# Kernel optimization log

Hardware: AMD Instinct MI355X
Metric: run time of the kernel (lower is better)

Reference implementation:

```python
import jax, jax.numpy as jnp
import numpy as np

B, D, M = 512, 1024, 32768
K, MULTI_K, AUX_K = 32, 128, 64
DEAD_THRESH = 256
MATRYOSHKA_SIZES = [4096, 16384, 32768]


def setup_inputs() -> dict:
    key = jax.random.key(0)
    k0, k1, k2, k3, k4, k5 = jax.random.split(key, 6)
    return {
        "x": jax.random.normal(k0, (B, D), dtype=jnp.float32),
        "W_enc": jax.random.normal(k1, (M, D), dtype=jnp.float32) * 0.02,
        "W_dec": jax.random.normal(k2, (D, M), dtype=jnp.float32) * 0.02,
        "input_bias": jax.random.normal(k3, (D,), dtype=jnp.float32) * 0.01,
        "neuron_bias": jax.random.normal(k4, (M,), dtype=jnp.float32) * 0.01,
        "steps_since_activation": jax.random.randint(k5, (M,), 0, 512, dtype=jnp.int64),
    }


def reference(x, W_enc, W_dec, input_bias, neuron_bias, steps_since_activation):
    xc = x - input_bias                                   # [B, D]
    pre_act = xc @ W_enc.T + neuron_bias                  # [B, M]

    topk_values, topk_indices = jax.lax.top_k(pre_act, K)
    topk_values = jax.nn.relu(topk_values)
    multik_values, multik_indices = jax.lax.top_k(pre_act, MULTI_K)
    multik_values = jax.nn.relu(multik_values)

    rows = jnp.arange(pre_act.shape[0])[:, None]
    activations = jnp.zeros_like(pre_act).at[rows, topk_indices].set(topk_values)
    multik_activations = jnp.zeros_like(pre_act).at[rows, multik_indices].set(multik_values)

    reconstruction = activations @ W_dec.T + input_bias
    multik_reconstruction = multik_activations @ W_dec.T + input_bias

    # matryoshka partial reconstructions (all sizes except the last/full one)
    neuron_ids = jnp.arange(M)
    matryoshka_recons = []
    for m_i in MATRYOSHKA_SIZES[:-1]:
        partial_acts = activations * (neuron_ids < m_i).astype(activations.dtype)
        matryoshka_recons.append(partial_acts @ W_dec.T + input_bias)

    # aux-k over dead neurons (steps incremented by 1 before the mask in torch)
    dead_mask = ((steps_since_activation + 1) > DEAD_THRESH).astype(pre_act.dtype)
    aux_values, aux_indices = jax.lax.top_k(pre_act * dead_mask, AUX_K)
    aux_values = jax.nn.relu(aux_values)

    return (reconstruction, multik_reconstruction,
            matryoshka_recons[0], matryoshka_recons[1],
            topk_indices, topk_values, aux_indices, aux_values)
```

## Files before the change

kernel.cpp:

```cpp
#include <hip/hip_runtime.h>
#include <stdint.h>

#define B_ 512
#define D_ 1024
#define M_ 32768

typedef _Float16 half8 __attribute__((ext_vector_type(8)));
typedef _Float16 half4 __attribute__((ext_vector_type(4)));
typedef float f32x4 __attribute__((ext_vector_type(4)));

__device__ __forceinline__ unsigned f2k(float f) {
    unsigned b = __float_as_uint(f);
    return (b & 0x80000000u) ? ~b : (b | 0x80000000u);
}
__device__ __forceinline__ float k2f(unsigned k) {
    unsigned b = (k & 0x80000000u) ? (k & 0x7FFFFFFFu) : ~k;
    return __uint_as_float(b);
}
__device__ __forceinline__ unsigned long long d2k(double d) {
    unsigned long long b = (unsigned long long)__double_as_longlong(d);
    return (b & 0x8000000000000000ull) ? ~b : (b | 0x8000000000000000ull);
}

__device__ __forceinline__ void gld16(const void* g, void* l) {
    __builtin_amdgcn_global_load_lds(
        (__attribute__((address_space(1))) void*)(uintptr_t)g,
        (__attribute__((address_space(3))) void*)(unsigned)(uintptr_t)l,
        16, 0, 0);
}

__global__ __launch_bounds__(256) void split_x_k(
    const float* __restrict__ x, const float* __restrict__ ib,
    _Float16* __restrict__ xh)
{
    int i = blockIdx.x * 256 + threadIdx.x;
    float4 v = ((const float4*)x)[i];
    float4 bb = ((const float4*)ib)[i & 255];
    float a0 = (v.x - bb.x) * 2048.0f;
    float a1 = (v.y - bb.y) * 2048.0f;
    float a2 = (v.z - bb.z) * 2048.0f;
    float a3 = (v.w - bb.w) * 2048.0f;
    half4 hv = {(_Float16)a0, (_Float16)a1, (_Float16)a2, (_Float16)a3};
    ((half4*)xh)[i] = hv;
}

__global__ __launch_bounds__(256, 3) void enc_tr(
    const _Float16* __restrict__ xhf,
    const float* __restrict__ wenc, const float* __restrict__ nb,
    _Float16* __restrict__ preact,
    const float* __restrict__ wdec, _Float16* __restrict__ wdt)
{
    __shared__ alignas(16) char smem[32768];

    const int tid = threadIdx.x;
    const int chunk = blockIdx.x >> 8;

    if (chunk % 3 != 0) {
        const int sub = (chunk - 1 - chunk / 3) * 256 + (blockIdx.x & 255);
        float* tile = (float*)smem;
        const int r = tid >> 2;
        const int q4 = (tid & 3) * 16;
        for (int s = 0; s < 4; ++s) {
            int tix = sub * 4 + s;
            int x0 = (tix & 511) * 64;
            int y0 = (tix >> 9) * 64;
            const float* src = wdec + (size_t)(y0 + r) * M_ + x0 + q4;
            float4 v0 = *(const float4*)(src + 0);
            float4 v1 = *(const float4*)(src + 4);
            float4 v2 = *(const float4*)(src + 8);
            float4 v3 = *(const float4*)(src + 12);
            float* dst = &tile[r * 65 + q4];
            dst[0] = v0.x;  dst[1] = v0.y;  dst[2] = v0.z;  dst[3] = v0.w;
            dst[4] = v1.x;  dst[5] = v1.y;  dst[6] = v1.z;  dst[7] = v1.w;
            dst[8] = v2.x;  dst[9] = v2.y;  dst[10] = v2.z; dst[11] = v2.w;
            dst[12] = v3.x; dst[13] = v3.y; dst[14] = v3.z; dst[15] = v3.w;
            __syncthreads();
            half8 h0, h1;
#pragma unroll
            for (int i = 0; i < 8; ++i) h0[i] = (_Float16)tile[(q4 + i) * 65 + r];
#pragma unroll
            for (int i = 0; i < 8; ++i) h1[i] = (_Float16)tile[(q4 + 8 + i) * 65 + r];
            _Float16* od = wdt + (size_t)(x0 + r) * D_ + y0 + q4;
            *(half8*)(od + 0) = h0;
            *(half8*)(od + 8) = h1;
            __syncthreads();
        }
        return;
    }

    _Float16* lA0 = (_Float16*)smem;
    _Float16* lB0 = (_Float16*)(smem + 16384);

    const int sub = (chunk / 3) * 256 + (blockIdx.x & 255);
    const int lane = tid & 63;
    const int wv = tid >> 6;
    const int wvr = wv >> 1;
    const int wvc = wv & 1;

    const int lb = sub >> 3;
    const int j0 = ((sub & 7) * 32 + (lb >> 2)) * 128;
    const int i0 = (lb & 3) * 128;

    const int ln15 = lane & 15;
    const int kq = (lane >> 4) * 8;

    f32x4 acc1[4][4];
#pragma unroll
    for (int r = 0; r < 4; ++r)
#pragma unroll
        for (int c = 0; c < 4; ++c)
            acc1[r][c] = (f32x4){0.f, 0.f, 0.f, 0.f};

    const int o0 = tid * 16;
    const int o1 = o0 + 4096;
    const int rA0 = o0 >> 6, rA1 = o1 >> 6;
    const int cA0s = (o0 & 63) ^ (((rA0 >> 1) & 3) << 4);
    const int cA1s = (o1 & 63) ^ (((rA1 >> 1) & 3) << 4);

    const int rW = tid >> 1;
    const int c16 = (tid & 1) * 16;
    const int sw = ((rW >> 1) & 3) << 3;
    const int g0 = c16 ^ sw;
    const int g1 = (c16 + 8) ^ sw;

    const int rowA = wvr * 64 + ln15;
    const int rowB = wvc * 64 + ln15;

#define STAGEA(k0, s)                                                                      \
    do {                                                                                   \
        gld16((const char*)(xhf + (size_t)(i0 + rA0) * 1024 + (k0)) + cA0s, (char*)lA0 + (s) * 8192 + o0); \
        gld16((const char*)(xhf + (size_t)(i0 + rA1) * 1024 + (k0)) + cA1s, (char*)lA0 + (s) * 8192 + o1); \
    } while (0)

#define LOADB(k0)                                                                          \
    do {                                                                                   \
        const float* wp = wenc + (size_t)(j0 + rW) * 1024 + (k0) + c16;                    \
        wv0 = *(const float4*)wp;                                                          \
        wv1 = *(const float4*)(wp + 4);                                                    \
        wv2 = *(const float4*)(wp + 8);                                                    \
        wv3 = *(const float4*)(wp + 12);                                                   \
    } while (0)

#define WRITEB(s)                                                                          \
    do {                                                                                   \
        half8 b0, b1;                                                                      \
        b0[0] = (_Float16)(wv0.x * 2048.0f); b0[1] = (_Float16)(wv0.y * 2048.0f);          \
        b0[2] = (_Float16)(wv0.z * 2048.0f); b0[3] = (_Float16)(wv0.w * 2048.0f);          \
        b0[4] = (_Float16)(wv1.x * 2048.0f); b0[5] = (_Float16)(wv1.y * 2048.0f);          \
        b0[6] = (_Float16)(wv1.z * 2048.0f); b0[7] = (_Float16)(wv1.w * 2048.0f);          \
        b1[0] = (_Float16)(wv2.x * 2048.0f); b1[1] = (_Float16)(wv2.y * 2048.0f);          \
        b1[2] = (_Float16)(wv2.z * 2048.0f); b1[3] = (_Float16)(wv2.w * 2048.0f);          \
        b1[4] = (_Float16)(wv3.x * 2048.0f); b1[5] = (_Float16)(wv3.y * 2048.0f);          \
        b1[6] = (_Float16)(wv3.z * 2048.0f); b1[7] = (_Float16)(wv3.w * 2048.0f);          \
        *(half8*)&lB0[(s) * 4096 + rW * 32 + g0] = b0;                                     \
        *(half8*)&lB0[(s) * 4096 + rW * 32 + g1] = b1;                                     \
    } while (0)

    float4 wv0, wv1, wv2, wv3;
    LOADB(0);
    asm volatile("s_waitcnt vmcnt(0)" ::: "memory");
    WRITEB(0);
    STAGEA(0, 0);
    LOADB(32);
    STAGEA(32, 1);
    asm volatile("s_waitcnt vmcnt(2)" ::: "memory");
    WRITEB(1);
    asm volatile("s_waitcnt lgkmcnt(0)" ::: "memory");
    __builtin_amdgcn_s_barrier();

    int cur = 0;
    for (int k0 = 0; k0 < 1024; k0 += 32) {
        if (k0 + 64 < 1024) LOADB(k0 + 64);

        half8 aH[4], bH[4];
#pragma unroll
        for (int r = 0; r < 4; ++r) {
            const int ra = rowA + r * 16;
            const int ka = kq ^ (((ra >> 1) & 3) << 3);
            aH[r] = *(const half8*)&lA0[cur * 4096 + ra * 32 + ka];
        }
#pragma unroll
        for (int c = 0; c < 4; ++c) {
            const int rb = rowB + c * 16;
            const int kb = kq ^ (((rb >> 1) & 3) << 3);
            bH[c] = *(const half8*)&lB0[cur * 4096 + rb * 32 + kb];
        }
#pragma unroll
        for (int r = 0; r < 4; ++r)
#pragma unroll
            for (int c = 0; c < 4; ++c)
                acc1[r][c] = __builtin_amdgcn_mfma_f32_16x16x32_f16(aH[r], bH[c], acc1[r][c], 0, 0, 0);

        if (k0 + 32 < 1024) {
            asm volatile("s_waitcnt lgkmcnt(0)" ::: "memory");
            __builtin_amdgcn_s_barrier();

            if (k0 + 64 < 1024) {
                STAGEA(k0 + 64, cur);
                asm volatile("s_waitcnt vmcnt(2)" ::: "memory");
                WRITEB(cur);
            } else {
                asm volatile("s_waitcnt vmcnt(0)" ::: "memory");
            }
            asm volatile("s_waitcnt lgkmcnt(0)" ::: "memory");
            __builtin_amdgcn_s_barrier();
        }
        cur ^= 1;
    }
#undef STAGEA
#undef LOADB
#undef WRITEB

    asm volatile("s_waitcnt lgkmcnt(0)" ::: "memory");
    __builtin_amdgcn_s_barrier();
    _Float16* ct = (_Float16*)smem;
    const float s1 = 0x1p-22f;
#pragma unroll
    for (int c = 0; c < 4; ++c) {
        int n = wvc * 64 + c * 16 + ln15;
        float nbv = nb[j0 + n];
#pragma unroll
        for (int r = 0; r < 4; ++r) {
            int mb = wvr * 64 + r * 16 + (lane >> 4) * 4;
#pragma unroll
            for (int e = 0; e < 4; ++e)
                ct[(mb + e) * 128 + n] = (_Float16)(acc1[r][c][e] * s1 + nbv);
        }
    }
    __syncthreads();
#pragma unroll
    for (int s = 0; s < 8; ++s) {
        int idx = s * 256 + tid;
        int row = idx >> 4;
        int off8 = (idx & 15) * 8;
        *(half8*)(preact + (size_t)(i0 + row) * M_ + j0 + off8) = *(half8*)&ct[row * 128 + off8];
    }
}

__global__ __launch_bounds__(1024, 2) void selresdec(
    const _Float16* __restrict__ preact, const int* __restrict__ steps,
    const float* __restrict__ x, const float* __restrict__ ib,
    const float* __restrict__ wenc, const float* __restrict__ nb,
    const _Float16* __restrict__ wdt,
    float* __restrict__ out_tidx, float* __restrict__ out_tval,
    float* __restrict__ out_aidx, float* __restrict__ out_aval,
    float* __restrict__ o_recon, float* __restrict__ o_multik,
    float* __restrict__ o_mat0, float* __restrict__ o_mat1)
{
    __shared__ unsigned histU[4096];
    __shared__ unsigned histM[4096];
    __shared__ unsigned coarseU[256];
    __shared__ unsigned coarseM[256];
    __shared__ unsigned long long candU[512];
    __shared__ unsigned long long candM[512];
    __shared__ double xcs[1024];
    __shared__ double part[128][8];
    __shared__ unsigned long long kU[64];
    __shared__ unsigned long long kM[128];
    __shared__ float vU[64];
    __shared__ float vM[128];
    __shared__ int sidx[128];
    __shared__ float sval[128];
    __shared__ int auxm[80];
    __shared__ int ridx[32];
    __shared__ float rval[32];
    __shared__ unsigned cntU, cntM, thrU, thrM, cbU, cbM, cumU, cumM;

    const int t = threadIdx.x;
    const int b = blockIdx.x;
    const half8* rowh = (const half8*)(preact + (size_t)b * M_);

    for (int i = t; i < 4096; i += 1024) { histU[i] = 0; histM[i] = 0; }
    if (t < 512) { candU[t] = 0ULL; candM[t] = 0ULL; }
    if (t == 0) { cntU = 0; cntM = 0; }
    xcs[t] = (double)x[(size_t)b * 1024 + t] - (double)ib[t];
    if (t < 64)  { kU[t] = 0ULL; vU[t] = 0.f; }
    if (t < 128) { kM[t] = 0ULL; vM[t] = 0.f; }
    __syncthreads();

    unsigned deadmask = 0;
#pragma unroll
    for (int p = 0; p < 4; ++p) {
        int base = 2 * t + 2048 * p;
        int4 s0 = ((const int4*)steps)[base];
        int4 s1 = ((const int4*)steps)[base + 1];
        unsigned mb = 0;
        if (s0.x + 1 > 256) mb |= 1u;
        if (s0.y + 1 > 256) mb |= 2u;
        if (s0.z + 1 > 256) mb |= 4u;
        if (s0.w + 1 > 256) mb |= 8u;
        if (s1.x + 1 > 256) mb |= 16u;
        if (s1.y + 1 > 256) mb |= 32u;
        if (s1.z + 1 > 256) mb |= 64u;
        if (s1.w + 1 > 256) mb |= 128u;
        deadmask |= mb << (p * 8);
    }

    half8 v[4];
#pragma unroll
    for (int p = 0; p < 4; ++p) {
        v[p] = rowh[t + p * 1024];
#pragma unroll
        for (int e = 0; e < 8; ++e) {
            float val = (float)v[p][e];
            if (val > 0.f) {
                unsigned key = f2k(val) >> 20;
                atomicAdd(&histU[key], 1u);
                if ((deadmask >> (p * 8 + e)) & 1u) atomicAdd(&histM[key], 1u);
            }
        }
    }
    __syncthreads();

    if (t < 256) {
        unsigned s = 0;
#pragma unroll
        for (int j = 0; j < 16; ++j) s += histU[t * 16 + j];
        coarseU[t] = s;
    } else if (t < 512) {
        int c = t - 256;
        unsigned s = 0;
#pragma unroll
        for (int j = 0; j < 16; ++j) s += histM[c * 16 + j];
        coarseM[c] = s;
    }
    __syncthreads();

    for (int off = 1; off < 256; off <<= 1) {
        unsigned xv = 0;
        if (t < 256)      xv = coarseU[t] + (t + off < 256 ? coarseU[t + off] : 0u);
        else if (t < 512) { int c = t - 256; xv = coarseM[c] + (c + off < 256 ? coarseM[c + off] : 0u); }
        __syncthreads();
        if (t < 256)      coarseU[t] = xv;
        else if (t < 512) coarseM[t - 256] = xv;
        __syncthreads();
    }

    if (t < 256) {
        unsigned S = coarseU[t];
        unsigned Sn = (t < 255) ? coarseU[t + 1] : 0u;
        if (S >= 128u && (t == 255 || Sn < 128u)) { cbU = (unsigned)t; cumU = Sn; }
    } else if (t < 512) {
        int c = t - 256;
        unsigned S = coarseM[c];
        unsigned Sn = (c < 255) ? coarseM[c + 1] : 0u;
        if (S >= 64u && (c == 255 || Sn < 64u)) { cbM = (unsigned)c; cumM = Sn; }
        if (c == 0 && S < 64u) { cbM = 0u; cumM = Sn; }
    }
    __syncthreads();

    if (t == 0) {
        unsigned cum = cumU;
        int base = (int)cbU * 16, tb = base;
        for (int f = base + 15; f >= base; --f) {
            unsigned h = histU[f];
            if (cum + h >= 128u) { tb = f; break; }
            cum += h;
        }
        thrU = (unsigned)tb;
    }
    if (t == 64) {
        unsigned cum = cumM;
        int base = (int)cbM * 16, tb = base;
        for (int f = base + 15; f >= base; --f) {
            unsigned h = histM[f];
            if (cum + h >= 64u) { tb = f; break; }
            cum += h;
        }
        thrM = (unsigned)(tb > 0 ? tb - 1 : 0);
    }
    __syncthreads();

    const unsigned TU = thrU, TM = thrM;

#pragma unroll
    for (int p = 0; p < 4; ++p) {
#pragma unroll
        for (int e = 0; e < 8; ++e) {
            float val = (float)v[p][e];
            unsigned key = f2k(val);
            int m = (t + p * 1024) * 8 + e;
            if ((key >> 20) >= TU) {
                unsigned pz = atomicAdd(&cntU, 1u);
                if (pz < 512u) candU[pz] = ((unsigned long long)key << 32) | (unsigned)(~m);
            }
            if (((deadmask >> (p * 8 + e)) & 1u) && (key >> 20) >= TM) {
                unsigned pz = atomicAdd(&cntM, 1u);
                if (pz < 512u) candM[pz] = ((unsigned long long)key << 32) | (unsigned)(~m);
            }
        }
    }
    __syncthreads();

    {
        unsigned long long* arr = (t < 512) ? candU : candM;
        const unsigned i = (unsigned)t & 511u;
        for (unsigned kk = 2; kk <= 512; kk <<= 1) {
            for (unsigned j = kk >> 1; j > 0; j >>= 1) {
                unsigned ixj = i ^ j;
                if (ixj > i) {
                    bool desc = ((i & kk) == 0);
                    unsigned long long a = arr[i], c = arr[ixj];
                    if (desc ? (a < c) : (a > c)) { arr[i] = c; arr[ixj] = a; }
                }
                unsigned nj = (j > 1) ? (j >> 1) : ((kk << 1) <= 512u ? kk : 0u);
                if (j >= 64 || nj >= 64) __syncthreads();
                else asm volatile("s_waitcnt lgkmcnt(0)" ::: "memory");
            }
        }
    }
    __syncthreads();

    if (t < 128) {
        unsigned long long c = candU[t];
        unsigned m = ~(unsigned)c;
        float vv = k2f((unsigned)(c >> 32));
        sidx[t] = (int)m;
        sval[t] = vv > 0.f ? vv : 0.f;
    }
    if (t < 80) {
        unsigned long long c = candM[t];
        auxm[t] = c ? (int)(~(unsigned)c) : -1;
    }
    __syncthreads();

    {
        const int ci = t >> 3, q = t & 7;
        int m = (ci < 48) ? sidx[ci] : auxm[ci - 48];
        if (m >= 0) {
            const float* w = wenc + (size_t)m * 1024 + q * 128;
            const double* xq = xcs + q * 128;
            double a0 = 0.0, a1 = 0.0, a2 = 0.0, a3 = 0.0;
            for (int d = 0; d < 128; d += 4) {
                float4 wv = *(const float4*)(w + d);
                a0 = fma((double)wv.x, xq[d + 0], a0);
                a1 = fma((double)wv.y, xq[d + 1], a1);
                a2 = fma((double)wv.z, xq[d + 2], a2);
                a3 = fma((double)wv.w, xq[d + 3], a3);
            }
            part[ci][q] = ((a0 + a1) + (a2 + a3));
        }
    }
    __syncthreads();

    if (t < 128) {
        int m = (t < 48) ? sidx[t] : auxm[t - 48];
        if (m >= 0) {
            double vd = (((part[t][0] + part[t][1]) + (part[t][2] + part[t][3]))
                       + ((part[t][4] + part[t][5]) + (part[t][6] + part[t][7])))
                      + (double)nb[m];
            unsigned long long key = (d2k(vd) & 0xFFFFFFFFFFFF0000ull)
                                   | (unsigned long long)((~(unsigned)m) & 0xFFFFu);
            float vf = (float)vd;
            if (t < 48) { kU[t] = key; vU[t] = vf; }
            else        { kM[t - 48] = key; vM[t - 48] = vf; }
        }
    }
    __syncthreads();

    for (unsigned kk = 2; kk <= 128; kk <<= 1) {
        for (unsigned j = kk >> 1; j > 0; j >>= 1) {
            unsigned i = (unsigned)t, ixj = i ^ j;
            if (kk <= 64 && i < 64 && ixj > i) {
                bool desc = ((i & kk) == 0);
                unsigned long long a = kU[i], c = kU[ixj];
                if (desc ? (a < c) : (a > c)) {
                    kU[i] = c; kU[ixj] = a;
                    float fa = vU[i]; vU[i] = vU[ixj]; vU[ixj] = fa;
                }
            }
            if (i < 128 && ixj > i) {
                bool desc = ((i & kk) == 0);
                unsigned long long a = kM[i], c = kM[ixj];
                if (desc ? (a < c) : (a > c)) {
                    kM[i] = c; kM[ixj] = a;
                    float fa = vM[i]; vM[i] = vM[ixj]; vM[ixj] = fa;
                }
            }
            __syncthreads();
        }
    }

    if (t < 32) {
        unsigned mm = (~(unsigned)kU[t]) & 0xFFFFu;
        float vv = vU[t];
        float rv = vv > 0.f ? vv : 0.f;
        ridx[t] = (int)mm;
        rval[t] = rv;
        out_tidx[b * 32 + t] = (float)mm;
        out_tval[b * 32 + t] = rv;
    }
    if (t < 64) {
        unsigned mm = (~(unsigned)kM[t]) & 0xFFFFu;
        float vv = vM[t];
        out_aidx[b * 64 + t] = (float)mm;
        out_aval[b * 64 + t] = vv > 0.f ? vv : 0.f;
    }
    __syncthreads();

    {
        const int d = t;
        float bias = ib[d];
        float mul = bias, rec = bias, m0 = bias, m1 = bias;
        for (int k = 0; k < 128; ++k) {
            float vv = sval[k];
            float w = (float)wdt[(size_t)sidx[k] * D_ + d];
            mul += vv * w;
        }
        for (int k = 0; k < 32; ++k) {
            int idx = ridx[k];
            float vv = rval[k];
            float w = (float)wdt[(size_t)idx * D_ + d];
            rec += vv * w;
            if (idx < 16384) {
                m1 += vv * w;
                if (idx < 4096) m0 += vv * w;
            }
        }
        size_t o = (size_t)b * D_ + d;
        o_recon[o]  = rec;
        o_multik[o] = mul;
        o_mat0[o]   = m0;
        o_mat1[o]   = m1;
    }
}

extern "C" void kernel_launch(void* const* d_in, const int* in_sizes, int n_in,
                              void* d_out, int out_size, void* d_ws, size_t ws_size,
                              hipStream_t stream)
{
    const float* x     = (const float*)d_in[0];
    const float* wenc  = (const float*)d_in[1];
    const float* wdec  = (const float*)d_in[2];
    const float* ib    = (const float*)d_in[3];
    const float* nb    = (const float*)d_in[4];
    const int*   steps = (const int*)d_in[5];
    float* out = (float*)d_out;

    char* ws = (char*)d_ws;
    _Float16*  preact  = (_Float16*)ws;
    _Float16*  wdt     = (_Float16*)(ws + 67108864);
    _Float16*  xhf     = (_Float16*)(ws + 201326592);

    float* out_recon  = out;
    float* out_multik = out + 524288;
    float* out_mat0   = out + 1048576;
    float* out_mat1   = out + 1572864;
    float* out_tidx   = out + 2097152;
    float* out_tval   = out + 2097152 + 16384;
    float* out_aidx   = out + 2097152 + 32768;
    float* out_aval   = out + 2097152 + 32768 + 32768;

    split_x_k<<<dim3(512), dim3(256), 0, stream>>>(x, ib, xhf);
    enc_tr<<<dim3(3072), dim3(256), 0, stream>>>(xhf, wenc, nb, preact, wdec, wdt);
    selresdec<<<dim3(512), dim3(1024), 0, stream>>>(
        preact, steps, x, ib, wenc, nb, wdt,
        out_tidx, out_tval, out_aidx, out_aval,
        out_recon, out_multik, out_mat0, out_mat1);
}
```

Before: 452.1 us.

## Fuse x centering and fp16 cast into encoder GEMM; reuse multik loads for top-k decode

Removes the separate split_x_k kernel: the encoder GEMM now loads fp32 x and input_bias directly, subtracts, scales and converts to fp16 while staging the A tile into LDS, replacing the async global-to-LDS loads of a precomputed fp16 buffer. In the decode stage, the top-32 reconstruction no longer does its own 32 W_dec row gathers. Each top-k entry is flagged inside the first 48 entries of the sorted multi-k list, so those weight loads are shared with the multi-k accumulation. This saves a launch and a 32-row gather per column, but adds per-iteration fp32 x loads and conversion inside the GEMM. It also assumes every top-32 index appears among the first 48 multi-k entries, which could break on ties.

```diff
diff --git a/kernel.cpp b/kernel.cpp
--- a/kernel.cpp
+++ b/kernel.cpp
@@ -22,30 +22,8 @@
     return (b & 0x8000000000000000ull) ? ~b : (b | 0x8000000000000000ull);
 }
 
-__device__ __forceinline__ void gld16(const void* g, void* l) {
-    __builtin_amdgcn_global_load_lds(
-        (__attribute__((address_space(1))) void*)(uintptr_t)g,
-        (__attribute__((address_space(3))) void*)(unsigned)(uintptr_t)l,
-        16, 0, 0);
-}
-
-__global__ __launch_bounds__(256) void split_x_k(
+__global__ __launch_bounds__(256, 3) void enc_tr(
     const float* __restrict__ x, const float* __restrict__ ib,
-    _Float16* __restrict__ xh)
-{
-    int i = blockIdx.x * 256 + threadIdx.x;
-    float4 v = ((const float4*)x)[i];
-    float4 bb = ((const float4*)ib)[i & 255];
-    float a0 = (v.x - bb.x) * 2048.0f;
-    float a1 = (v.y - bb.y) * 2048.0f;
-    float a2 = (v.z - bb.z) * 2048.0f;
-    float a3 = (v.w - bb.w) * 2048.0f;
-    half4 hv = {(_Float16)a0, (_Float16)a1, (_Float16)a2, (_Float16)a3};
-    ((half4*)xh)[i] = hv;
-}
-
-__global__ __launch_bounds__(256, 3) void enc_tr(
-    const _Float16* __restrict__ xhf,
     const float* __restrict__ wenc, const float* __restrict__ nb,
     _Float16* __restrict__ preact,
     const float* __restrict__ wdec, _Float16* __restrict__ wdt)
@@ -111,12 +89,6 @@
         for (int c = 0; c < 4; ++c)
             acc1[r][c] = (f32x4){0.f, 0.f, 0.f, 0.f};
 
-    const int o0 = tid * 16;
-    const int o1 = o0 + 4096;
-    const int rA0 = o0 >> 6, rA1 = o1 >> 6;
-    const int cA0s = (o0 & 63) ^ (((rA0 >> 1) & 3) << 4);
-    const int cA1s = (o1 & 63) ^ (((rA1 >> 1) & 3) << 4);
-
     const int rW = tid >> 1;
     const int c16 = (tid & 1) * 16;
     const int sw = ((rW >> 1) & 3) << 3;
@@ -126,14 +98,13 @@
     const int rowA = wvr * 64 + ln15;
     const int rowB = wvc * 64 + ln15;
 
-#define STAGEA(k0, s)                                                                      \
+#define LOADAB(k0)                                                                         \
     do {                                                                                   \
-        gld16((const char*)(xhf + (size_t)(i0 + rA0) * 1024 + (k0)) + cA0s, (char*)lA0 + (s) * 8192 + o0); \
-        gld16((const char*)(xhf + (size_t)(i0 + rA1) * 1024 + (k0)) + cA1s, (char*)lA0 + (s) * 8192 + o1); \
-    } while (0)
-
-#define LOADB(k0)                                                                          \
-    do {                                                                                   \
+        const float* xp = x + (size_t)(i0 + rW) * 1024 + (k0) + c16;                       \
+        xv0 = *(const float4*)xp;                                                          \
+        xv1 = *(const float4*)(xp + 4);                                                    \
+        xv2 = *(const float4*)(xp + 8);                                                    \
+        xv3 = *(const float4*)(xp + 12);                                                   \
         const float* wp = wenc + (size_t)(j0 + rW) * 1024 + (k0) + c16;                    \
         wv0 = *(const float4*)wp;                                                          \
         wv1 = *(const float4*)(wp + 4);                                                    \
@@ -141,9 +112,28 @@
         wv3 = *(const float4*)(wp + 12);                                                   \
     } while (0)
 
-#define WRITEB(s)                                                                          \
+#define LOADIB(k0)                                                                         \
     do {                                                                                   \
-        half8 b0, b1;                                                                      \
+        const float* ip = ib + (k0) + c16;                                                 \
+        iv0 = *(const float4*)ip;                                                          \
+        iv1 = *(const float4*)(ip + 4);                                                    \
+        iv2 = *(const float4*)(ip + 8);                                                    \
+        iv3 = *(const float4*)(ip + 12);                                                   \
+    } while (0)
+
+#define WRITEAB(s)                                                                         \
+    do {                                                                                   \
+        half8 a0, a1, b0, b1;                                                              \
+        a0[0] = (_Float16)((xv0.x - iv0.x) * 2048.0f); a0[1] = (_Float16)((xv0.y - iv0.y) * 2048.0f); \
+        a0[2] = (_Float16)((xv0.z - iv0.z) * 2048.0f); a0[3] = (_Float16)((xv0.w - iv0.w) * 2048.0f); \
+        a0[4] = (_Float16)((xv1.x - iv1.x) * 2048.0f); a0[5] = (_Float16)((xv1.y - iv1.y) * 2048.0f); \
+        a0[6] = (_Float16)((xv1.z - iv1.z) * 2048.0f); a0[7] = (_Float16)((xv1.w - iv1.w) * 2048.0f); \
+        a1[0] = (_Float16)((xv2.x - iv2.x) * 2048.0f); a1[1] = (_Float16)((xv2.y - iv2.y) * 2048.0f); \
+        a1[2] = (_Float16)((xv2.z - iv2.z) * 2048.0f); a1[3] = (_Float16)((xv2.w - iv2.w) * 2048.0f); \
+        a1[4] = (_Float16)((xv3.x - iv3.x) * 2048.0f); a1[5] = (_Float16)((xv3.y - iv3.y) * 2048.0f); \
+        a1[6] = (_Float16)((xv3.z - iv3.z) * 2048.0f); a1[7] = (_Float16)((xv3.w - iv3.w) * 2048.0f); \
+        *(half8*)&lA0[(s) * 4096 + rW * 32 + g0] = a0;                                     \
+        *(half8*)&lA0[(s) * 4096 + rW * 32 + g1] = a1;                                     \
         b0[0] = (_Float16)(wv0.x * 2048.0f); b0[1] = (_Float16)(wv0.y * 2048.0f);          \
         b0[2] = (_Float16)(wv0.z * 2048.0f); b0[3] = (_Float16)(wv0.w * 2048.0f);          \
         b0[4] = (_Float16)(wv1.x * 2048.0f); b0[5] = (_Float16)(wv1.y * 2048.0f);          \
@@ -156,21 +146,21 @@
         *(half8*)&lB0[(s) * 4096 + rW * 32 + g1] = b1;                                     \
     } while (0)
 
-    float4 wv0, wv1, wv2, wv3;
-    LOADB(0);
+    float4 xv0, xv1, xv2, xv3, wv0, wv1, wv2, wv3, iv0, iv1, iv2, iv3;
+    LOADAB(0);
+    LOADIB(0);
     asm volatile("s_waitcnt vmcnt(0)" ::: "memory");
-    WRITEB(0);
-    STAGEA(0, 0);
-    LOADB(32);
-    STAGEA(32, 1);
-    asm volatile("s_waitcnt vmcnt(2)" ::: "memory");
-    WRITEB(1);
+    WRITEAB(0);
+    LOADAB(32);
+    LOADIB(32);
+    asm volatile("s_waitcnt vmcnt(0)" ::: "memory");
+    WRITEAB(1);
     asm volatile("s_waitcnt lgkmcnt(0)" ::: "memory");
     __builtin_amdgcn_s_barrier();
 
     int cur = 0;
     for (int k0 = 0; k0 < 1024; k0 += 32) {
-        if (k0 + 64 < 1024) LOADB(k0 + 64);
+        if (k0 + 64 < 1024) LOADAB(k0 + 64);
 
         half8 aH[4], bH[4];
 #pragma unroll
@@ -196,20 +186,18 @@
             __builtin_amdgcn_s_barrier();
 
             if (k0 + 64 < 1024) {
-                STAGEA(k0 + 64, cur);
-                asm volatile("s_waitcnt vmcnt(2)" ::: "memory");
-                WRITEB(cur);
-            } else {
+                LOADIB(k0 + 64);
                 asm volatile("s_waitcnt vmcnt(0)" ::: "memory");
+                WRITEAB(cur);
             }
             asm volatile("s_waitcnt lgkmcnt(0)" ::: "memory");
             __builtin_amdgcn_s_barrier();
         }
         cur ^= 1;
     }
-#undef STAGEA
-#undef LOADB
-#undef WRITEB
+#undef LOADAB
+#undef LOADIB
+#undef WRITEAB
 
     asm volatile("s_waitcnt lgkmcnt(0)" ::: "memory");
     __builtin_amdgcn_s_barrier();
@@ -262,8 +250,8 @@
     __shared__ int sidx[128];
     __shared__ float sval[128];
     __shared__ int auxm[80];
-    __shared__ int ridx[32];
-    __shared__ float rval[32];
+    __shared__ unsigned tflag[48];
+    __shared__ float trv[48];
     __shared__ unsigned cntU, cntM, thrU, thrM, cbU, cbM, cumU, cumM;
 
     const int t = threadIdx.x;
@@ -276,6 +264,7 @@
     xcs[t] = (double)x[(size_t)b * 1024 + t] - (double)ib[t];
     if (t < 64)  { kU[t] = 0ULL; vU[t] = 0.f; }
     if (t < 128) { kM[t] = 0ULL; vM[t] = 0.f; }
+    if (t < 48)  { tflag[t] = 0u; trv[t] = 0.f; }
     __syncthreads();
 
     unsigned deadmask = 0;
@@ -485,10 +474,10 @@
         unsigned mm = (~(unsigned)kU[t]) & 0xFFFFu;
         float vv = vU[t];
         float rv = vv > 0.f ? vv : 0.f;
-        ridx[t] = (int)mm;
-        rval[t] = rv;
         out_tidx[b * 32 + t] = (float)mm;
         out_tval[b * 32 + t] = rv;
+        for (int j = 0; j < 48; ++j)
+            if (sidx[j] == (int)mm) { tflag[j] = 1u; trv[j] = rv; }
     }
     if (t < 64) {
         unsigned mm = (~(unsigned)kM[t]) & 0xFFFFu;
@@ -506,15 +495,14 @@
             float vv = sval[k];
             float w = (float)wdt[(size_t)sidx[k] * D_ + d];
             mul += vv * w;
-        }
-        for (int k = 0; k < 32; ++k) {
-            int idx = ridx[k];
-            float vv = rval[k];
-            float w = (float)wdt[(size_t)idx * D_ + d];
-            rec += vv * w;
-            if (idx < 16384) {
-                m1 += vv * w;
-                if (idx < 4096) m0 += vv * w;
+            if (k < 48 && tflag[k]) {
+                float rvv = trv[k];
+                int idx = sidx[k];
+                rec += rvv * w;
+                if (idx < 16384) {
+                    m1 += rvv * w;
+                    if (idx < 4096) m0 += rvv * w;
+                }
             }
         }
         size_t o = (size_t)b * D_ + d;
@@ -540,7 +528,6 @@
     char* ws = (char*)d_ws;
     _Float16*  preact  = (_Float16*)ws;
     _Float16*  wdt     = (_Float16*)(ws + 67108864);
-    _Float16*  xhf     = (_Float16*)(ws + 201326592);
 
     float* out_recon  = out;
     float* out_multik = out + 524288;
@@ -551,8 +538,7 @@
     float* out_aidx   = out + 2097152 + 32768;
     float* out_aval   = out + 2097152 + 32768 + 32768;
 
-    split_x_k<<<dim3(512), dim3(256), 0, stream>>>(x, ib, xhf);
-    enc_tr<<<dim3(3072), dim3(256), 0, stream>>>(xhf, wenc, nb, preact, wdec, wdt);
+    enc_tr<<<dim3(3072), dim3(256), 0, stream>>>(x, ib, wenc, nb, preact, wdec, wdt);
     selresdec<<<dim3(512), dim3(1024), 0, stream>>>(
         preact, steps, x, ib, wenc, nb, wdt,
         out_tidx, out_tval, out_aidx, out_aval,
```

Measured after the change: 516.4 us. 14.2% more time.
